# Kernel tuning notes

Hardware: AMD Instinct MI355X
Metric: run time of the kernel (lower is better)

The kernel has to match this reference:

```python
import jax, jax.numpy as jnp
from jax import lax
import numpy as np

PATCH = 8


def setup_inputs() -> dict:
    key = jax.random.key(0)
    ks = jax.random.split(key, 6)
    B, C, H, W = 8, 128, 256, 256
    half = C // 2
    x = jax.random.normal(ks[0], (B, C, H, W), dtype=jnp.float32)
    # nn.Parameter(torch.randn(...)) -> unit normal real spectral filter
    fft_filt = jax.random.normal(ks[1], (C, PATCH, PATCH // 2 + 1), dtype=jnp.float32)
    w_in = jax.random.normal(ks[2], (C, C), dtype=jnp.float32) * 0.05
    w_before = jax.random.normal(ks[3], (half, half), dtype=jnp.float32) * 0.05
    w_dw = jax.random.normal(ks[4], (half, 1, 3, 3), dtype=jnp.float32) * 0.05
    w_out = jax.random.normal(ks[5], (C, half), dtype=jnp.float32) * 0.05
    return {"x": x, "fft_filt": fft_filt, "w_in": w_in,
            "w_before": w_before, "w_dw": w_dw, "w_out": w_out}


def reference(x, fft_filt, w_in, w_before, w_dw, w_out):
    B, C, H, W = x.shape
    p = PATCH
    pad_h = (p - H % p) % p
    pad_w = (p - W % p) % p
    xp = jnp.pad(x, ((0, 0), (0, 0), (0, pad_h), (0, pad_w))) if (pad_h or pad_w) else x
    Hp, Wp = H + pad_h, W + pad_w
    h, w = Hp // p, Wp // p

    # project_in: 1x1 conv, no bias
    y = jnp.einsum('bchw,oc->bohw', xp, w_in)

    # b c (h p1) (w p2) -> b h w c p1 p2
    yp = y.reshape(B, C, h, p, w, p).transpose(0, 2, 4, 1, 3, 5)
    yf = jnp.fft.rfft2(yp)                      # complex, last-two-axes FFT of 8x8 patches
    yf = yf * fft_filt                          # real filter broadcast over (b,h,w)
    yi = jnp.fft.irfft2(yf, s=(p, p))
    # b h w c p1 p2 -> b c (h p1) (w p2)
    y = yi.transpose(0, 3, 1, 4, 2, 5).reshape(B, C, Hp, Wp)

    # chunk + gated GELU (torch default gelu = exact erf)
    x1, x2 = jnp.split(y, 2, axis=1)
    g = jax.nn.gelu(x1, approximate=False) * x2

    # before_dwconv: 1x1 conv on half channels
    g = jnp.einsum('bchw,oc->bohw', g, w_before)
    # depthwise 3x3, padding 1
    g = lax.conv_general_dilated(g, w_dw, window_strides=(1, 1), padding='SAME',
                                 feature_group_count=C // 2,
                                 dimension_numbers=('NCHW', 'OIHW', 'NCHW'))
    # project_out: 1x1 conv half -> dim
    out = jnp.einsum('bchw,oc->bohw', g, w_out)
    out = out[:, :, :H, :W]
    return out + x
```

## Files before the change

### kernel.cpp

```cpp
#include <hip/hip_runtime.h>
#include <math.h>

#define BB 8
#define CC 128
#define HH 256
#define WW 256
#define PLANE (HH * WW)

__global__ __launch_bounds__(256) void prep_kernel(
    const float* __restrict__ filt, const float* __restrict__ w_in,
    const float* __restrict__ w_before, const float* __restrict__ w_out,
    float* __restrict__ kkt, float* __restrict__ w_in_t,
    float* __restrict__ w_before_t, float* __restrict__ w_out_t) {
  int idx = blockIdx.x * 256 + threadIdx.x;
  if (idx < 8192) {
    int c = idx >> 6;
    int un = idx & 63;
    int u = un >> 3, n = un & 7;
    const float cs8[8] = {1.f,  0.70710678118654752f,  0.f, -0.70710678118654752f,
                          -1.f, -0.70710678118654752f, 0.f, 0.70710678118654752f};
    float s = 0.f;
#pragma unroll
    for (int p = 0; p < 8; ++p) {
#pragma unroll
      for (int q = 0; q < 5; ++q) {
        float m = (q == 0 || q == 4) ? 1.f : 2.f;
        s += m * filt[(c * 8 + p) * 5 + q] * cs8[(p * u + q * n) & 7];
      }
    }
    kkt[un * 128 + c] = s * (1.f / 64.f);
  } else if (idx < 24576) {
    int j = idx - 8192;
    int o = j >> 7, c = j & 127;
    w_in_t[c * 128 + o] = w_in[o * 128 + c];
  } else if (idx < 28672) {
    int j = idx - 24576;
    int o = j >> 6, c = j & 63;
    w_before_t[c * 64 + o] = w_before[o * 64 + c];
  } else if (idx < 36864) {
    int j = idx - 28672;
    int o = j >> 6, c = j & 63;
    w_out_t[c * 128 + o] = w_out[o * 64 + c];
  }
}

__global__ __launch_bounds__(256) void fused1_kernel(
    const float* __restrict__ x, const float* __restrict__ w_in_t,
    const float* __restrict__ w_before_t, const float* __restrict__ kkt,
    float* __restrict__ g2) {
  __shared__ float buf[128 * 64];

  int bid = blockIdx.x;
  int b = bid >> 10;
  int py = (bid >> 5) & 31;
  int px = bid & 31;
  int h0 = py * 8, w0 = px * 8;
  int t = threadIdx.x;
  const float* xb = x + (size_t)b * CC * PLANE;

#pragma unroll
  for (int i = 0; i < 8; ++i) {
    int f = t + 256 * i;
    int r = f >> 1;
    int k4 = f & 1;
    int c = r >> 3, ph = r & 7;
    float4 v = *(const float4*)(xb + (size_t)c * PLANE +
                                (size_t)(h0 + ph) * WW + w0 + k4 * 4);
    *(float4*)(buf + c * 64 + ph * 8 + k4 * 4) = v;
  }
  __syncthreads();

  int ob = t >> 3;
  int pb = t & 7;

  float acc[4][8];
#pragma unroll
  for (int i = 0; i < 4; ++i)
#pragma unroll
    for (int j = 0; j < 8; ++j) acc[i][j] = 0.f;

  const float* wp = w_in_t + ob * 4;
  const float* bp = buf + pb * 8;
#pragma unroll 4
  for (int c = 0; c < 128; ++c) {
    float4 lo = *(const float4*)(bp + c * 64);
    float4 hi = *(const float4*)(bp + c * 64 + 4);
    float4 wv = *(const float4*)(wp + c * 128);
    float xv[8] = {lo.x, lo.y, lo.z, lo.w, hi.x, hi.y, hi.z, hi.w};
    float wa[4] = {wv.x, wv.y, wv.z, wv.w};
#pragma unroll
    for (int i = 0; i < 4; ++i)
#pragma unroll
      for (int j = 0; j < 8; ++j) acc[i][j] += wa[i] * xv[j];
  }

  float acc2[4][8];
#pragma unroll
  for (int i = 0; i < 4; ++i)
#pragma unroll
    for (int j = 0; j < 8; ++j) acc2[i][j] = 0.f;

  float r8[4][8];
#pragma unroll
  for (int i = 0; i < 4; ++i)
#pragma unroll
    for (int j = 0; j < 8; ++j) r8[i][j] = acc[i][j];

  const float* kb = kkt + ob * 4;
  int srcm1 = (t & 56) | ((t - 1) & 7);
#pragma unroll
  for (int s = 0; s < 8; ++s) {
    if (s > 0) {
#pragma unroll
      for (int i = 0; i < 4; ++i)
#pragma unroll
        for (int j = 0; j < 8; ++j) r8[i][j] = __shfl(r8[i][j], srcm1, 64);
    }
#pragma unroll
    for (int tt = 0; tt < 8; ++tt) {
      float4 kv = *(const float4*)(kb + (s * 8 + tt) * 128);
      float ka[4] = {kv.x, kv.y, kv.z, kv.w};
#pragma unroll
      for (int i = 0; i < 4; ++i)
#pragma unroll
        for (int j = 0; j < 8; ++j)
          acc2[i][j] += ka[i] * r8[i][(j - tt) & 7];
    }
  }
  __syncthreads();

#pragma unroll
  for (int i = 0; i < 4; ++i) {
    float* dst = buf + (ob * 4 + i) * 64 + pb * 8;
    *(float4*)dst = make_float4(acc2[i][0], acc2[i][1], acc2[i][2], acc2[i][3]);
    *(float4*)(dst + 4) =
        make_float4(acc2[i][4], acc2[i][5], acc2[i][6], acc2[i][7]);
  }
  __syncthreads();

#pragma unroll
  for (int it = 0; it < 16; ++it) {
    int f = t + it * 256;
    float a = buf[f];
    float g = buf[f + 4096];
    float ge = 0.5f * a * (1.f + erff(a * 0.70710678118654752f));
    buf[f] = ge * g;
  }
  __syncthreads();

  float acc3[2][8];
#pragma unroll
  for (int i = 0; i < 2; ++i)
#pragma unroll
    for (int j = 0; j < 8; ++j) acc3[i][j] = 0.f;

  const float* wbp = w_before_t + ob * 2;
#pragma unroll 4
  for (int c = 0; c < 64; ++c) {
    float4 lo = *(const float4*)(bp + c * 64);
    float4 hi = *(const float4*)(bp + c * 64 + 4);
    float2 wv = *(const float2*)(wbp + c * 64);
    float gv[8] = {lo.x, lo.y, lo.z, lo.w, hi.x, hi.y, hi.z, hi.w};
#pragma unroll
    for (int j = 0; j < 8; ++j) {
      acc3[0][j] += wv.x * gv[j];
      acc3[1][j] += wv.y * gv[j];
    }
  }

  size_t obase = (size_t)b * 64 * PLANE + (size_t)(h0 + pb) * WW + w0;
#pragma unroll
  for (int i = 0; i < 2; ++i) {
    int o = ob * 2 + i;
    float* dst = g2 + obase + (size_t)o * PLANE;
    *(float4*)dst = make_float4(acc3[i][0], acc3[i][1], acc3[i][2], acc3[i][3]);
    *(float4*)(dst + 4) =
        make_float4(acc3[i][4], acc3[i][5], acc3[i][6], acc3[i][7]);
  }
}

__global__ __launch_bounds__(256) void dwconv_kernel(
    const float* __restrict__ g2, const float* __restrict__ w_dw,
    float* __restrict__ dout) {
  int wseg = blockIdx.x;
  int hseg = blockIdx.y;
  int bc = blockIdx.z;
  int c = bc & 63;
  const float* src = g2 + (size_t)bc * PLANE;
  float* dst = dout + (size_t)bc * PLANE;
  __shared__ float tile[34][66];
  int w0 = wseg * 64, h0 = hseg * 32;
  int t = threadIdx.x;
  for (int f = t; f < 34 * 66; f += 256) {
    int r = f / 66, cl = f - r * 66;
    int hh = h0 + r - 1, ww = w0 + cl - 1;
    float v = 0.f;
    if (hh >= 0 && hh < HH && ww >= 0 && ww < WW) v = src[hh * WW + ww];
    tile[r][cl] = v;
  }
  float k9[9];
#pragma unroll
  for (int i = 0; i < 9; ++i) k9[i] = w_dw[c * 9 + i];
  __syncthreads();
  int cl = t & 63;
#pragma unroll
  for (int rep = 0; rep < 8; ++rep) {
    int r = rep * 4 + (t >> 6);
    float s = 0.f;
#pragma unroll
    for (int i = 0; i < 3; ++i)
#pragma unroll
      for (int j = 0; j < 3; ++j) s += k9[i * 3 + j] * tile[r + i][cl + j];
    dst[(size_t)(h0 + r) * WW + w0 + cl] = s;
  }
}

__global__ __launch_bounds__(256) void mixout_kernel(
    const float* __restrict__ d, const float* __restrict__ w_out_t,
    const float* __restrict__ x, float* __restrict__ out) {
  int bid = blockIdx.x;
  int wseg = bid & 3;
  int hh = (bid >> 2) & 255;
  int b = bid >> 10;
  __shared__ float ds[64 * 64];
  int t = threadIdx.x;
  const float* dbase = d + (size_t)b * 64 * PLANE + (size_t)hh * WW + wseg * 64;
#pragma unroll
  for (int i = 0; i < 4; ++i) {
    int f = t + 256 * i;
    int c = f >> 4, k4 = f & 15;
    *(float4*)(ds + c * 64 + k4 * 4) =
        *(const float4*)(dbase + (size_t)c * PLANE + k4 * 4);
  }
  __syncthreads();

  int og = __builtin_amdgcn_readfirstlane(t >> 6);
  int pix = t & 63;
  float acc[32];
#pragma unroll
  for (int i = 0; i < 32; ++i) acc[i] = 0.f;

  const float* wt = w_out_t + og * 32;
#pragma unroll 2
  for (int c = 0; c < 64; ++c) {
    float xv = ds[c * 64 + pix];
#pragma unroll
    for (int i = 0; i < 32; ++i) acc[i] += wt[c * 128 + i] * xv;
  }

  size_t pbase =
      (size_t)b * CC * PLANE + (size_t)hh * WW + (size_t)wseg * 64 + pix;
#pragma unroll
  for (int i = 0; i < 32; ++i) {
    int o = og * 32 + i;
    out[pbase + (size_t)o * PLANE] = acc[i] + x[pbase + (size_t)o * PLANE];
  }
}

extern "C" void kernel_launch(void* const* d_in, const int* in_sizes, int n_in,
                              void* d_out, int out_size, void* d_ws,
                              size_t ws_size, hipStream_t stream) {
  const float* x = (const float*)d_in[0];
  const float* fft_filt = (const float*)d_in[1];
  const float* w_in = (const float*)d_in[2];
  const float* w_before = (const float*)d_in[3];
  const float* w_dw = (const float*)d_in[4];
  const float* w_out = (const float*)d_in[5];
  float* out = (float*)d_out;

  char* ws = (char*)d_ws;
  float* kkt = (float*)ws;
  float* w_in_t = kkt + 8192;
  float* w_before_t = w_in_t + 16384;
  float* w_out_t = w_before_t + 4096;
  float* g2 = (float*)(ws + (1 << 20));
  float* dbuf = g2 + (size_t)BB * 64 * PLANE;

  hipLaunchKernelGGL(prep_kernel, dim3(144), dim3(256), 0, stream, fft_filt,
                     w_in, w_before, w_out, kkt, w_in_t, w_before_t, w_out_t);
  hipLaunchKernelGGL(fused1_kernel, dim3(8192), dim3(256), 0, stream, x,
                     w_in_t, w_before_t, kkt, g2);
  hipLaunchKernelGGL(dwconv_kernel, dim3(4, 8, 512), dim3(256), 0, stream, g2,
                     w_dw, dbuf);
  hipLaunchKernelGGL(mixout_kernel, dim3(8192), dim3(256), 0, stream, dbuf,
                     w_out_t, x, out);
}
```

Measured before the change: 1.256 ms.

## Run fused1 1x1 convs on bf16x3 split MFMA with transposed LDS reads

Replaces the scalar FP32 project_in and before_dwconv matmuls in fused1 with MFMA 16x16x32 bf16 instructions. Precision is kept close to FP32 by splitting each operand into high and low bf16 parts and summing three products. Activations are staged in LDS in a swizzled bf16 layout and fed to the MFMAs through ds_read_b64_tr_b16. The patch-FFT step now reads shifted rows from padded LDS instead of using cross-lane shuffles. This adds conversion work, larger shared memory use (about 50KB, which may lower occupancy), and explicit waitcnt barriers that serialize LDS reads against the MFMAs.

```diff
diff --git a/kernel.cpp b/kernel.cpp
--- a/kernel.cpp
+++ b/kernel.cpp
@@ -1,17 +1,45 @@
 #include <hip/hip_runtime.h>
 #include <math.h>
+#include <stdint.h>
 
 #define BB 8
 #define CC 128
 #define HH 256
 #define WW 256
 #define PLANE (HH * WW)
+#define YSTR 68
+
+typedef __attribute__((ext_vector_type(8))) short short8;
+typedef __attribute__((ext_vector_type(4))) float f32x4;
+typedef __attribute__((ext_vector_type(2))) int i32x2;
+
+__device__ __forceinline__ unsigned short f2bf(float f) {
+  unsigned u = __float_as_uint(f);
+  u += 0x7FFFu + ((u >> 16) & 1u);
+  return (unsigned short)(u >> 16);
+}
+__device__ __forceinline__ float bf2f(unsigned short h) {
+  return __uint_as_float(((unsigned)h) << 16);
+}
+
+__device__ __forceinline__ i32x2 tr16(uint32_t addr) {
+  i32x2 d;
+  asm volatile("ds_read_b64_tr_b16 %0, %1" : "=v"(d) : "v"(addr));
+  return d;
+}
+__device__ __forceinline__ short8 mk8(i32x2 a, i32x2 b) {
+  union { i32x2 d[2]; short8 s; } u;
+  u.d[0] = a; u.d[1] = b;
+  return u.s;
+}
 
 __global__ __launch_bounds__(256) void prep_kernel(
     const float* __restrict__ filt, const float* __restrict__ w_in,
     const float* __restrict__ w_before, const float* __restrict__ w_out,
-    float* __restrict__ kkt, float* __restrict__ w_in_t,
-    float* __restrict__ w_before_t, float* __restrict__ w_out_t) {
+    float* __restrict__ kkt, unsigned short* __restrict__ w_in_h,
+    unsigned short* __restrict__ w_in_l,
+    unsigned short* __restrict__ w_before_h,
+    unsigned short* __restrict__ w_before_l, float* __restrict__ w_out_t) {
   int idx = blockIdx.x * 256 + threadIdx.x;
   if (idx < 8192) {
     int c = idx >> 6;
@@ -31,12 +59,16 @@
     kkt[un * 128 + c] = s * (1.f / 64.f);
   } else if (idx < 24576) {
     int j = idx - 8192;
-    int o = j >> 7, c = j & 127;
-    w_in_t[c * 128 + o] = w_in[o * 128 + c];
+    float f = w_in[j];
+    unsigned short h = f2bf(f);
+    w_in_h[j] = h;
+    w_in_l[j] = f2bf(f - bf2f(h));
   } else if (idx < 28672) {
     int j = idx - 24576;
-    int o = j >> 6, c = j & 63;
-    w_before_t[c * 64 + o] = w_before[o * 64 + c];
+    float f = w_before[j];
+    unsigned short h = f2bf(f);
+    w_before_h[j] = h;
+    w_before_l[j] = f2bf(f - bf2f(h));
   } else if (idx < 36864) {
     int j = idx - 28672;
     int o = j >> 6, c = j & 63;
@@ -45,93 +77,145 @@
 }
 
 __global__ __launch_bounds__(256) void fused1_kernel(
-    const float* __restrict__ x, const float* __restrict__ w_in_t,
-    const float* __restrict__ w_before_t, const float* __restrict__ kkt,
-    float* __restrict__ g2) {
-  __shared__ float buf[128 * 64];
+    const float* __restrict__ x, const unsigned short* __restrict__ w_in_h,
+    const unsigned short* __restrict__ w_in_l,
+    const unsigned short* __restrict__ w_before_h,
+    const unsigned short* __restrict__ w_before_l,
+    const float* __restrict__ kkt, float* __restrict__ g2) {
+  __shared__ __align__(16) char smem[51200];
+  unsigned short* xh = (unsigned short*)smem;
+  unsigned short* xl = (unsigned short*)(smem + 16384);
+  float* yb = (float*)smem;
+  unsigned short* gh = (unsigned short*)(smem + 34816);
+  unsigned short* gl = (unsigned short*)(smem + 43008);
 
   int bid = blockIdx.x;
   int b = bid >> 10;
   int py = (bid >> 5) & 31;
-  int px = bid & 31;
-  int h0 = py * 8, w0 = px * 8;
+  int pxb = bid & 31;
+  int h0 = py * 8, w0 = pxb * 8;
   int t = threadIdx.x;
   const float* xb = x + (size_t)b * CC * PLANE;
 
 #pragma unroll
-  for (int i = 0; i < 8; ++i) {
-    int f = t + 256 * i;
-    int r = f >> 1;
-    int k4 = f & 1;
-    int c = r >> 3, ph = r & 7;
-    float4 v = *(const float4*)(xb + (size_t)c * PLANE +
-                                (size_t)(h0 + ph) * WW + w0 + k4 * 4);
-    *(float4*)(buf + c * 64 + ph * 8 + k4 * 4) = v;
-  }
+  for (int it = 0; it < 4; ++it) {
+    int oc = t + it * 256;
+    int c = oc >> 3, ph = oc & 7;
+    const float* src = xb + (size_t)c * PLANE + (size_t)(h0 + ph) * WW + w0;
+    float4 v0 = *(const float4*)src;
+    float4 v1 = *(const float4*)(src + 4);
+    float v[8] = {v0.x, v0.y, v0.z, v0.w, v1.x, v1.y, v1.z, v1.w};
+    unsigned hu[4], lu[4];
+#pragma unroll
+    for (int q = 0; q < 4; ++q) {
+      unsigned short ha = f2bf(v[2 * q]), hb = f2bf(v[2 * q + 1]);
+      unsigned short la = f2bf(v[2 * q] - bf2f(ha));
+      unsigned short lb = f2bf(v[2 * q + 1] - bf2f(hb));
+      hu[q] = (unsigned)ha | ((unsigned)hb << 16);
+      lu[q] = (unsigned)la | ((unsigned)lb << 16);
+    }
+    int ks = c >> 5, wc = c & 31;
+    int blk = (wc >> 2) & 1, sg = wc >> 3, jj = wc & 3;
+    int nt = ph >> 1, colh = ph & 1;
+    int e = ((ks * 4 + nt) * 2 + blk) * 256 + (sg * 4 + jj) * 16 + colh * 8;
+    *(uint4*)(xh + e) = make_uint4(hu[0], hu[1], hu[2], hu[3]);
+    *(uint4*)(xl + e) = make_uint4(lu[0], lu[1], lu[2], lu[3]);
+  }
+  __syncthreads();
+
+  int l = t & 63;
+  int wv = t >> 6;
+  int l15 = l & 15, l4 = l >> 4;
+  uint32_t trbase =
+      (uint32_t)(uintptr_t)smem + (uint32_t)(l15 * 2 + l4 * 128);
+
+  f32x4 zero4 = {0.f, 0.f, 0.f, 0.f};
+  f32x4 acc[2][4];
+#pragma unroll
+  for (int mt = 0; mt < 2; ++mt)
+#pragma unroll
+    for (int nt = 0; nt < 4; ++nt) acc[mt][nt] = zero4;
+
+#pragma unroll
+  for (int ks = 0; ks < 4; ++ks) {
+    short8 ah[2], al[2];
+#pragma unroll
+    for (int mt = 0; mt < 2; ++mt) {
+      int o = wv * 32 + mt * 16 + l15;
+      ah[mt] = *(const short8*)(w_in_h + o * 128 + ks * 32 + l4 * 8);
+      al[mt] = *(const short8*)(w_in_l + o * 128 + ks * 32 + l4 * 8);
+    }
+#pragma unroll
+    for (int nt = 0; nt < 4; ++nt) {
+      uint32_t base = trbase + (uint32_t)((ks * 4 + nt) * 1024);
+      i32x2 h0v = tr16(base);
+      i32x2 h1v = tr16(base + 512);
+      i32x2 l0v = tr16(base + 16384);
+      i32x2 l1v = tr16(base + 16384 + 512);
+      asm volatile("s_waitcnt lgkmcnt(0)" ::: "memory");
+      __builtin_amdgcn_sched_barrier(0);
+      short8 bh = mk8(h0v, h1v);
+      short8 bl = mk8(l0v, l1v);
+#pragma unroll
+      for (int mt = 0; mt < 2; ++mt) {
+        acc[mt][nt] = __builtin_amdgcn_mfma_f32_16x16x32_bf16(
+            ah[mt], bh, acc[mt][nt], 0, 0, 0);
+        acc[mt][nt] = __builtin_amdgcn_mfma_f32_16x16x32_bf16(
+            ah[mt], bl, acc[mt][nt], 0, 0, 0);
+        acc[mt][nt] = __builtin_amdgcn_mfma_f32_16x16x32_bf16(
+            al[mt], bh, acc[mt][nt], 0, 0, 0);
+      }
+    }
+  }
+  __syncthreads();
+
+#pragma unroll
+  for (int mt = 0; mt < 2; ++mt)
+#pragma unroll
+    for (int nt = 0; nt < 4; ++nt)
+#pragma unroll
+      for (int r = 0; r < 4; ++r) {
+        int o = wv * 32 + mt * 16 + l4 * 4 + r;
+        yb[o * YSTR + nt * 16 + l15] = acc[mt][nt][r];
+      }
   __syncthreads();
 
   int ob = t >> 3;
   int pb = t & 7;
-
-  float acc[4][8];
+  float acc2[4][8];
 #pragma unroll
   for (int i = 0; i < 4; ++i)
 #pragma unroll
-    for (int j = 0; j < 8; ++j) acc[i][j] = 0.f;
-
-  const float* wp = w_in_t + ob * 4;
-  const float* bp = buf + pb * 8;
-#pragma unroll 4
-  for (int c = 0; c < 128; ++c) {
-    float4 lo = *(const float4*)(bp + c * 64);
-    float4 hi = *(const float4*)(bp + c * 64 + 4);
-    float4 wv = *(const float4*)(wp + c * 128);
-    float xv[8] = {lo.x, lo.y, lo.z, lo.w, hi.x, hi.y, hi.z, hi.w};
-    float wa[4] = {wv.x, wv.y, wv.z, wv.w};
-#pragma unroll
-    for (int i = 0; i < 4; ++i)
-#pragma unroll
-      for (int j = 0; j < 8; ++j) acc[i][j] += wa[i] * xv[j];
-  }
-
-  float acc2[4][8];
-#pragma unroll
-  for (int i = 0; i < 4; ++i)
-#pragma unroll
     for (int j = 0; j < 8; ++j) acc2[i][j] = 0.f;
 
-  float r8[4][8];
-#pragma unroll
-  for (int i = 0; i < 4; ++i)
-#pragma unroll
-    for (int j = 0; j < 8; ++j) r8[i][j] = acc[i][j];
-
-  const float* kb = kkt + ob * 4;
-  int srcm1 = (t & 56) | ((t - 1) & 7);
 #pragma unroll
   for (int s = 0; s < 8; ++s) {
-    if (s > 0) {
+    int r = (pb - s) & 7;
+    float yr[4][8];
+#pragma unroll
+    for (int i = 0; i < 4; ++i) {
+      const float* p = yb + (ob * 4 + i) * YSTR + r * 8;
+      float4 v0 = *(const float4*)p;
+      float4 v1 = *(const float4*)(p + 4);
+      yr[i][0] = v0.x; yr[i][1] = v0.y; yr[i][2] = v0.z; yr[i][3] = v0.w;
+      yr[i][4] = v1.x; yr[i][5] = v1.y; yr[i][6] = v1.z; yr[i][7] = v1.w;
+    }
+#pragma unroll
+    for (int tt = 0; tt < 8; ++tt) {
+      float4 kv = *(const float4*)(kkt + (s * 8 + tt) * 128 + ob * 4);
+      float ka[4] = {kv.x, kv.y, kv.z, kv.w};
 #pragma unroll
       for (int i = 0; i < 4; ++i)
 #pragma unroll
-        for (int j = 0; j < 8; ++j) r8[i][j] = __shfl(r8[i][j], srcm1, 64);
-    }
-#pragma unroll
-    for (int tt = 0; tt < 8; ++tt) {
-      float4 kv = *(const float4*)(kb + (s * 8 + tt) * 128);
-      float ka[4] = {kv.x, kv.y, kv.z, kv.w};
-#pragma unroll
-      for (int i = 0; i < 4; ++i)
-#pragma unroll
         for (int j = 0; j < 8; ++j)
-          acc2[i][j] += ka[i] * r8[i][(j - tt) & 7];
+          acc2[i][j] += ka[i] * yr[i][(j - tt) & 7];
     }
   }
   __syncthreads();
 
 #pragma unroll
   for (int i = 0; i < 4; ++i) {
-    float* dst = buf + (ob * 4 + i) * 64 + pb * 8;
+    float* dst = yb + (ob * 4 + i) * YSTR + pb * 8;
     *(float4*)dst = make_float4(acc2[i][0], acc2[i][1], acc2[i][2], acc2[i][3]);
     *(float4*)(dst + 4) =
         make_float4(acc2[i][4], acc2[i][5], acc2[i][6], acc2[i][7]);
@@ -139,43 +223,91 @@
   __syncthreads();
 
 #pragma unroll
-  for (int it = 0; it < 16; ++it) {
-    int f = t + it * 256;
-    float a = buf[f];
-    float g = buf[f + 4096];
-    float ge = 0.5f * a * (1.f + erff(a * 0.70710678118654752f));
-    buf[f] = ge * g;
-  }
-  __syncthreads();
-
-  float acc3[2][8];
-#pragma unroll
-  for (int i = 0; i < 2; ++i)
-#pragma unroll
-    for (int j = 0; j < 8; ++j) acc3[i][j] = 0.f;
-
-  const float* wbp = w_before_t + ob * 2;
-#pragma unroll 4
-  for (int c = 0; c < 64; ++c) {
-    float4 lo = *(const float4*)(bp + c * 64);
-    float4 hi = *(const float4*)(bp + c * 64 + 4);
-    float2 wv = *(const float2*)(wbp + c * 64);
-    float gv[8] = {lo.x, lo.y, lo.z, lo.w, hi.x, hi.y, hi.z, hi.w};
-#pragma unroll
-    for (int j = 0; j < 8; ++j) {
-      acc3[0][j] += wv.x * gv[j];
-      acc3[1][j] += wv.y * gv[j];
-    }
-  }
-
-  size_t obase = (size_t)b * 64 * PLANE + (size_t)(h0 + pb) * WW + w0;
-#pragma unroll
-  for (int i = 0; i < 2; ++i) {
-    int o = ob * 2 + i;
-    float* dst = g2 + obase + (size_t)o * PLANE;
-    *(float4*)dst = make_float4(acc3[i][0], acc3[i][1], acc3[i][2], acc3[i][3]);
-    *(float4*)(dst + 4) =
-        make_float4(acc3[i][4], acc3[i][5], acc3[i][6], acc3[i][7]);
+  for (int it = 0; it < 2; ++it) {
+    int oc = t + it * 256;
+    int c = oc >> 3, ocl = oc & 7;
+    const float* pa = yb + c * YSTR + ocl * 8;
+    const float* pg = yb + (c + 64) * YSTR + ocl * 8;
+    float4 a0 = *(const float4*)pa, a1 = *(const float4*)(pa + 4);
+    float4 g0 = *(const float4*)pg, g1 = *(const float4*)(pg + 4);
+    float av[8] = {a0.x, a0.y, a0.z, a0.w, a1.x, a1.y, a1.z, a1.w};
+    float gv[8] = {g0.x, g0.y, g0.z, g0.w, g1.x, g1.y, g1.z, g1.w};
+    unsigned hu[4], lu[4];
+#pragma unroll
+    for (int q = 0; q < 4; ++q) {
+      float r0, r1;
+      {
+        float a = av[2 * q];
+        r0 = 0.5f * a * (1.f + erff(a * 0.70710678118654752f)) * gv[2 * q];
+      }
+      {
+        float a = av[2 * q + 1];
+        r1 = 0.5f * a * (1.f + erff(a * 0.70710678118654752f)) * gv[2 * q + 1];
+      }
+      unsigned short ha = f2bf(r0), hb = f2bf(r1);
+      unsigned short la = f2bf(r0 - bf2f(ha)), lb = f2bf(r1 - bf2f(hb));
+      hu[q] = (unsigned)ha | ((unsigned)hb << 16);
+      lu[q] = (unsigned)la | ((unsigned)lb << 16);
+    }
+    int ks = c >> 5, wc = c & 31;
+    int blk = (wc >> 2) & 1, sg = wc >> 3, jj = wc & 3;
+    int nt = ocl >> 1, colh = ocl & 1;
+    int e = ((ks * 4 + nt) * 2 + blk) * 256 + (sg * 4 + jj) * 16 + colh * 8;
+    *(uint4*)(gh + e) = make_uint4(hu[0], hu[1], hu[2], hu[3]);
+    *(uint4*)(gl + e) = make_uint4(lu[0], lu[1], lu[2], lu[3]);
+  }
+  __syncthreads();
+
+  f32x4 accd[4];
+#pragma unroll
+  for (int nt = 0; nt < 4; ++nt) accd[nt] = zero4;
+
+  uint32_t gtrbase = (uint32_t)(uintptr_t)smem + 34816u +
+                     (uint32_t)(l15 * 2 + l4 * 128);
+#pragma unroll
+  for (int ks = 0; ks < 2; ++ks) {
+    int o = wv * 16 + l15;
+    short8 wbh = *(const short8*)(w_before_h + o * 64 + ks * 32 + l4 * 8);
+    short8 wbl = *(const short8*)(w_before_l + o * 64 + ks * 32 + l4 * 8);
+#pragma unroll
+    for (int nt = 0; nt < 4; ++nt) {
+      uint32_t base = gtrbase + (uint32_t)((ks * 4 + nt) * 1024);
+      i32x2 h0v = tr16(base);
+      i32x2 h1v = tr16(base + 512);
+      i32x2 l0v = tr16(base + 8192);
+      i32x2 l1v = tr16(base + 8192 + 512);
+      asm volatile("s_waitcnt lgkmcnt(0)" ::: "memory");
+      __builtin_amdgcn_sched_barrier(0);
+      short8 bh = mk8(h0v, h1v);
+      short8 bl = mk8(l0v, l1v);
+      accd[nt] =
+          __builtin_amdgcn_mfma_f32_16x16x32_bf16(wbh, bh, accd[nt], 0, 0, 0);
+      accd[nt] =
+          __builtin_amdgcn_mfma_f32_16x16x32_bf16(wbh, bl, accd[nt], 0, 0, 0);
+      accd[nt] =
+          __builtin_amdgcn_mfma_f32_16x16x32_bf16(wbl, bh, accd[nt], 0, 0, 0);
+    }
+  }
+#pragma unroll
+  for (int nt = 0; nt < 4; ++nt)
+#pragma unroll
+    for (int r = 0; r < 4; ++r) {
+      int o = wv * 16 + l4 * 4 + r;
+      yb[o * YSTR + nt * 16 + l15] = accd[nt][r];
+    }
+  __syncthreads();
+
+#pragma unroll
+  for (int it = 0; it < 2; ++it) {
+    int oc = t + it * 256;
+    int o = oc >> 3, ocl = oc & 7;
+    const float* p = yb + o * YSTR + ocl * 8;
+    float4 v0 = *(const float4*)p;
+    float4 v1 = *(const float4*)(p + 4);
+    float* dst = g2 + (size_t)b * 64 * PLANE + (size_t)o * PLANE +
+                 (size_t)(h0 + ocl) * WW + w0;
+    *(float4*)dst = v0;
+    *(float4*)(dst + 4) = v1;
   }
 }
 
@@ -270,16 +402,19 @@
 
   char* ws = (char*)d_ws;
   float* kkt = (float*)ws;
-  float* w_in_t = kkt + 8192;
-  float* w_before_t = w_in_t + 16384;
-  float* w_out_t = w_before_t + 4096;
+  float* w_out_t = kkt + 8192;
+  unsigned short* w_in_h = (unsigned short*)(w_out_t + 8192);
+  unsigned short* w_in_l = w_in_h + 16384;
+  unsigned short* w_before_h = w_in_l + 16384;
+  unsigned short* w_before_l = w_before_h + 4096;
   float* g2 = (float*)(ws + (1 << 20));
   float* dbuf = g2 + (size_t)BB * 64 * PLANE;
 
   hipLaunchKernelGGL(prep_kernel, dim3(144), dim3(256), 0, stream, fft_filt,
-                     w_in, w_before, w_out, kkt, w_in_t, w_before_t, w_out_t);
+                     w_in, w_before, w_out, kkt, w_in_h, w_in_l, w_before_h,
+                     w_before_l, w_out_t);
   hipLaunchKernelGGL(fused1_kernel, dim3(8192), dim3(256), 0, stream, x,
-                     w_in_t, w_before_t, kkt, g2);
+                     w_in_h, w_in_l, w_before_h, w_before_l, kkt, g2);
   hipLaunchKernelGGL(dwconv_kernel, dim3(4, 8, 512), dim3(256), 0, stream, g2,
                      w_dw, dbuf);
   hipLaunchKernelGGL(mixout_kernel, dim3(8192), dim3(256), 0, stream, dbuf,
```

New measurement: 1.176 ms. 1.07x faster.
